# Kernel optimization log

Hardware: AMD Instinct MI355X
Metric: run time of the kernel (lower is better)

Reference implementation:

```python
import jax, jax.numpy as jnp
import numpy as np

SEQ = 2048
DIM = 2048
GROUPS = 8
GROUP_SIZE = 4
DQK = DIM // (GROUPS * GROUP_SIZE)  # 64 (also dim_v)


def _glorot(key, shape):
    # Faithful to source: dim_in = prod(shape[-1]) == shape[-1], so sigma = 1/sqrt(shape[-1])
    sigma = np.sqrt(2.0 / (shape[-1] + shape[-1])).astype(np.float32)
    return jax.random.normal(key, shape, dtype=jnp.float32) * sigma


def rope(x):
    """RoPE on last axis; x: [..., seq, dim]. Closed-form per-pair rotation."""
    seq, dim = x.shape[-2], x.shape[-1]
    half = dim // 2
    # angle[s, j] = s * 10000^(-2j/dim)
    inv_freq = 10000.0 ** (-2.0 * jnp.arange(half, dtype=jnp.float32) / dim)
    ang = jnp.arange(seq, dtype=jnp.float32)[:, None] * inv_freq[None, :]  # [seq, half]
    c, s = jnp.cos(ang), jnp.sin(ang)
    xp = x.reshape(*x.shape[:-1], half, 2)
    x1, x2 = xp[..., 0], xp[..., 1]
    out = jnp.stack([c * x1 - s * x2, s * x1 + c * x2], axis=-1)
    return out.reshape(x.shape)


def setup_inputs() -> dict:
    key = jax.random.key(0)
    kx, kq, kk, kv, ko = jax.random.split(key, 5)
    return {
        "x": jax.random.normal(kx, (SEQ, DIM), dtype=jnp.float32),
        "w_query": _glorot(kq, (GROUPS, GROUP_SIZE, DIM, DQK)),
        "w_key": _glorot(kk, (GROUPS, DIM, DQK)),
        "w_value": _glorot(kv, (GROUPS, DIM, DQK)),
        "w_out": _glorot(ko, (GROUPS, GROUP_SIZE, DQK, DIM)),
    }


def reference(x, w_query, w_key, w_value, w_out):
    seq = x.shape[0]
    dqk = w_query.shape[-1]
    # projections: g=groups, h=group_size (query heads per group)
    q = rope(jnp.einsum('sd,ghdk->ghsk', x, w_query))  # [g,h,seq,dqk]
    k = rope(jnp.einsum('sd,gdk->gsk', x, w_key))      # [g,seq,dqk]
    v = jnp.einsum('sd,gdv->gsv', x, w_value)          # [g,seq,dv]
    scores = jnp.einsum('ghsk,gtk->ghst', q, k) / jnp.sqrt(jnp.float32(dqk))
    causal = jnp.tril(jnp.ones((seq, seq), dtype=bool))  # log(tril(ones)) == 0 / -inf
    scores = jnp.where(causal, scores, -jnp.inf)
    probs = jax.nn.softmax(scores, axis=-1)
    o = jnp.einsum('ghst,gtv->ghsv', probs, v)
    # per-head out-proj then sum over (g, h)
    return jnp.einsum('ghsv,ghvd->sd', o, w_out)
```

## Files before the change

### kernel.cpp

```cpp
#include <hip/hip_runtime.h>
#include <hip/hip_bf16.h>

#define SEQ 2048
#define DIMM 2048
#define NQH 32
#define NKVH 8
#define HD 64

typedef _Float16 half8 __attribute__((ext_vector_type(8)));
typedef float f32x4 __attribute__((ext_vector_type(4)));
typedef __fp16 fp16raw2 __attribute__((ext_vector_type(2)));
using fp16 = _Float16;

typedef __attribute__((address_space(1))) unsigned int ga_u32;
typedef __attribute__((address_space(3))) unsigned int ls_u32;

__device__ __forceinline__ void gll16(const void* g, void* l) {
    __builtin_amdgcn_global_load_lds((const ga_u32*)g, (ls_u32*)l, 16, 0, 0);
}

__device__ __forceinline__ float fexp2(float x) {
#if __has_builtin(__builtin_amdgcn_exp2f)
    return __builtin_amdgcn_exp2f(x);
#else
    float r;
    asm("v_exp_f32 %0, %1" : "=v"(r) : "v"(x));
    return r;
#endif
}

__global__ void prep_kernel(const float* __restrict__ x,
                            const float* __restrict__ wq, const float* __restrict__ wk,
                            const float* __restrict__ wv, const float* __restrict__ wo,
                            fp16* __restrict__ xh, fp16* __restrict__ wqkvt,
                            fp16* __restrict__ w2t, float2* __restrict__ trig) {
    __shared__ float tile[64][65];
    const int bx = blockIdx.x;
    const int t = threadIdx.x;
    if (bx < 1024) {
#pragma unroll
        for (int it = 0; it < 4; it++) {
            int i = bx * 4096 + it * 1024 + t * 4;
            float4 v = *reinterpret_cast<const float4*>(x + i);
            fp16* o = xh + i;
            o[0] = (fp16)v.x; o[1] = (fp16)v.y; o[2] = (fp16)v.z; o[3] = (fp16)v.w;
        }
    } else if (bx < 2560) {
        const int zi = bx - 1024;
        const int z = zi >> 5;
        const int r0 = (zi & 31) * 64;
        const float* inh = (z < 32) ? wq + (size_t)z * SEQ * HD
                                    : (z < 40) ? wk + (size_t)(z - 32) * SEQ * HD
                                               : wv + (size_t)(z - 40) * SEQ * HD;
        fp16* outh = wqkvt + (size_t)z * HD * SEQ;
#pragma unroll
        for (int i = 0; i < 16; i++) {
            int idx = i * 256 + t;
            int r = idx >> 6, c = idx & 63;
            tile[r][c] = inh[(size_t)(r0 + r) * HD + c];
        }
        __syncthreads();
#pragma unroll
        for (int i = 0; i < 16; i++) {
            int idx = i * 256 + t;
            int cc = idx >> 6, rr = idx & 63;
            outh[(size_t)cc * SEQ + r0 + rr] = (fp16)tile[rr][cc];
        }
    } else if (bx < 3584) {
        const int zi = bx - 2560;
        const int r0 = (zi >> 5) * 64, c0 = (zi & 31) * 64;
#pragma unroll
        for (int i = 0; i < 16; i++) {
            int idx = i * 256 + t;
            int r = idx >> 6, c = idx & 63;
            tile[r][c] = wo[(size_t)(r0 + r) * 2048 + c0 + c];
        }
        __syncthreads();
#pragma unroll
        for (int i = 0; i < 16; i++) {
            int idx = i * 256 + t;
            int cc = idx >> 6, rr = idx & 63;
            w2t[(size_t)(c0 + cc) * 2048 + r0 + rr] = (fp16)tile[rr][cc];
        }
    } else {
        int idx = (bx - 3584) * 256 + t;
        int s = idx >> 5, j = idx & 31;
        float invf = expf(-0.28782313662425572f * (float)j);
        float sn, cs;
        sincosf((float)s * invf, &sn, &cs);
        trig[idx] = make_float2(cs, sn);
    }
}

__global__ __launch_bounds__(256) void gemm_qkv_fused(
    const fp16* __restrict__ A, const fp16* __restrict__ Bt, const float2* __restrict__ trig,
    fp16* __restrict__ qb, fp16* __restrict__ kb, fp16* __restrict__ vtb) {
    __shared__ fp16 As[2][64][64];
    __shared__ fp16 Bs[2][128][64];
    const int t = threadIdx.x;
    const int m0 = blockIdx.x * 64, n0 = blockIdx.y * 128;
    const int wid = t >> 6, lane = t & 63;
    const int wm = (wid >> 1) * 32, wn = (wid & 1) * 64;
    const int lr = lane & 15, lg = lane >> 4;
    f32x4 acc[2][4] = {};
    auto stage_ = [&](int kt, int b) {
#pragma unroll
        for (int s = t; s < 512; s += 256) {
            int row = s >> 3, ch = s & 7;
            int lch = ch ^ (row & 7);
            gll16(A + (size_t)(m0 + row) * 2048 + (kt << 6) + lch * 8,
                  (char*)&As[b][0][0] + s * 16);
        }
#pragma unroll
        for (int s = t; s < 1024; s += 256) {
            int row = s >> 3, ch = s & 7;
            int lch = ch ^ (row & 7);
            gll16(Bt + (size_t)(n0 + row) * 2048 + (kt << 6) + lch * 8,
                  (char*)&Bs[b][0][0] + s * 16);
        }
    };
    stage_(0, 0);
    __syncthreads();
    for (int kt = 0; kt < 32; ++kt) {
        const int cur = kt & 1;
        if (kt + 1 < 32) stage_(kt + 1, cur ^ 1);
#pragma unroll
        for (int kk = 0; kk < 2; kk++) {
            half8 af[2], bfv[4];
#pragma unroll
            for (int m = 0; m < 2; m++) {
                int row = wm + m * 16 + lr;
                af[m] = *(const half8*)((const char*)&As[cur][row][0] +
                                        (((kk * 4 + lg) ^ (row & 7)) * 16));
            }
#pragma unroll
            for (int n = 0; n < 4; n++) {
                int row = wn + n * 16 + lr;
                bfv[n] = *(const half8*)((const char*)&Bs[cur][row][0] +
                                         (((kk * 4 + lg) ^ (row & 7)) * 16));
            }
            __builtin_amdgcn_s_setprio(1);
#pragma unroll
            for (int m = 0; m < 2; m++)
#pragma unroll
                for (int n = 0; n < 4; n++)
                    acc[m][n] = __builtin_amdgcn_mfma_f32_16x16x32_f16(af[m], bfv[n], acc[m][n], 0, 0, 0);
            __builtin_amdgcn_s_setprio(0);
        }
        __syncthreads();
    }
    const int head0 = blockIdx.y * 2;
    if (head0 < 40) {
        const int head = head0 + (wid & 1);
        const float qscale = (head0 < 32) ? 0.18033688011112042f : 1.0f;
        fp16* outp = (head0 < 32) ? qb + (size_t)head * SEQ * HD
                                  : kb + (size_t)(head - 32) * SEQ * HD;
#pragma unroll
        for (int n = 0; n < 4; n++) {
            int c = n * 16 + lr;
            int j = c >> 1;
#pragma unroll
            for (int m = 0; m < 2; m++)
#pragma unroll
                for (int r = 0; r < 4; r++) {
                    int s = m0 + wm + m * 16 + lg * 4 + r;
                    float2 tc = trig[s * 32 + j];
                    float val = acc[m][n][r];
                    float pv = __shfl_xor(val, 1);
                    float o = (c & 1) ? (tc.y * pv + tc.x * val) : (tc.x * val - tc.y * pv);
                    outp[(size_t)s * HD + c] = (fp16)(o * qscale);
                }
        }
    } else {
        fp16* T = (fp16*)&Bs[0][0][0];
#pragma unroll
        for (int n = 0; n < 4; n++)
#pragma unroll
            for (int m = 0; m < 2; m++)
#pragma unroll
                for (int r = 0; r < 4; r++) {
                    int c = wn + n * 16 + lr;
                    int s = wm + m * 16 + lg * 4 + r;
                    T[c * 68 + s] = (fp16)acc[m][n][r];
                }
        __syncthreads();
        const int g0 = head0 - 40;
#pragma unroll
        for (int i = 0; i < 16; i++) {
            int idx = i * 256 + t;
            int c = idx >> 5, sp = (idx & 31) * 2;
            unsigned v = *(const unsigned*)&T[c * 68 + sp];
            *(unsigned*)(vtb + ((size_t)(g0 + (c >> 6)) * 64 + (c & 63)) * SEQ + m0 + sp) = v;
        }
    }
}

template <int BM, int BN, int WF32>
__global__ __launch_bounds__(256) void gemm_tpl(
    const fp16* __restrict__ A, const fp16* __restrict__ Bt, void* __restrict__ Cout, int Nout) {
    __shared__ fp16 As[2][BM][64];
    __shared__ fp16 Bs[2][BN][64];
    const int t = threadIdx.x;
    const int m0 = blockIdx.x * BM, n0 = blockIdx.y * BN;
    const int wid = t >> 6, lane = t & 63;
    const int wm = (wid >> 1) * (BM / 2), wn = (wid & 1) * (BN / 2);
    const int lr = lane & 15, lg = lane >> 4;
    constexpr int MR = BM / 32, NR = BN / 32;
    f32x4 acc[MR][NR] = {};
    auto stage_ = [&](int kt, int b) {
#pragma unroll
        for (int s = t; s < BM * 8; s += 256) {
            int row = s >> 3, ch = s & 7;
            int lch = ch ^ (row & 7);
            gll16(A + (size_t)(m0 + row) * 2048 + (kt << 6) + lch * 8,
                  (char*)&As[b][0][0] + s * 16);
        }
#pragma unroll
        for (int s = t; s < BN * 8; s += 256) {
            int row = s >> 3, ch = s & 7;
            int lch = ch ^ (row & 7);
            gll16(Bt + (size_t)(n0 + row) * 2048 + (kt << 6) + lch * 8,
                  (char*)&Bs[b][0][0] + s * 16);
        }
    };
    stage_(0, 0);
    __syncthreads();
    for (int kt = 0; kt < 32; ++kt) {
        const int cur = kt & 1;
        if (kt + 1 < 32) stage_(kt + 1, cur ^ 1);
#pragma unroll
        for (int kk = 0; kk < 2; kk++) {
            half8 af[MR], bfv[NR];
#pragma unroll
            for (int m = 0; m < MR; m++) {
                int row = wm + m * 16 + lr;
                af[m] = *(const half8*)((const char*)&As[cur][row][0] +
                                        (((kk * 4 + lg) ^ (row & 7)) * 16));
            }
#pragma unroll
            for (int n = 0; n < NR; n++) {
                int row = wn + n * 16 + lr;
                bfv[n] = *(const half8*)((const char*)&Bs[cur][row][0] +
                                         (((kk * 4 + lg) ^ (row & 7)) * 16));
            }
            __builtin_amdgcn_s_setprio(1);
#pragma unroll
            for (int m = 0; m < MR; m++)
#pragma unroll
                for (int n = 0; n < NR; n++)
                    acc[m][n] = __builtin_amdgcn_mfma_f32_16x16x32_f16(af[m], bfv[n], acc[m][n], 0, 0, 0);
            __builtin_amdgcn_s_setprio(0);
        }
        __syncthreads();
    }
#pragma unroll
    for (int m = 0; m < MR; m++)
#pragma unroll
        for (int n = 0; n < NR; n++)
#pragma unroll
            for (int r = 0; r < 4; r++) {
                int row = m0 + wm + m * 16 + lg * 4 + r;
                int col = n0 + wn + n * 16 + lr;
                if (WF32)
                    ((float*)Cout)[(size_t)row * Nout + col] = acc[m][n][r];
                else
                    ((fp16*)Cout)[(size_t)row * Nout + col] = (fp16)acc[m][n][r];
            }
}

__global__ __launch_bounds__(256) void attn_kernel(
    const fp16* __restrict__ qb, const fp16* __restrict__ kb,
    const fp16* __restrict__ vt, fp16* __restrict__ o_all) {
    __shared__ fp16 Kb[2][64][64];
    __shared__ fp16 Vb[2][64][64];
    __shared__ fp16 P[4][16][64];
    const int t = threadIdx.x, wid = t >> 6, lane = t & 63;
    const int bx = blockIdx.x;
    const int grp = bx >> 5;
    const int a = grp & 7;
    const int sel = grp >> 3;
    const int qt = (sel == 0) ? (31 - a) : (sel == 1) ? (8 + a) : (sel == 2) ? (23 - a) : a;
    const int head = bx & 31;
    const int g = head >> 2;
    const int lr = lane & 15, lg = lane >> 4;
    const fp16* qh = qb + (size_t)head * SEQ * HD;
    const fp16* kh = kb + (size_t)g * SEQ * HD;
    const fp16* vh = vt + (size_t)g * HD * SEQ;
    const int srow = lane >> 3, schunk = lane & 7;
    const int qr0 = qt * 64 + wid * 16;
    char* pb = (char*)&P[wid][0][0];

    half8 aq0 = *reinterpret_cast<const half8*>(qh + (size_t)(qr0 + lr) * HD + lg * 8);
    half8 aq1 = *reinterpret_cast<const half8*>(qh + (size_t)(qr0 + lr) * HD + 32 + lg * 8);
    f32x4 o[4] = {};
    float m_ = -1e30f, lsum_ = 0.0f;
    const int nt = qt + 1;

    const char* kga = (const char*)kh + (size_t)((wid * 16 + srow) * 64 + (schunk ^ srow) * 8) * 2;
    const char* vga = (const char*)vh + ((size_t)(wid * 16 + srow) * 2048 + (size_t)((schunk ^ srow) * 8)) * 2;
    char* kd0 = (char*)&Kb[0][wid * 16][0];
    char* vd0 = (char*)&Vb[0][wid * 16][0];
    int sb = 0;
    auto stage = [&]() {
        char* kdst = kd0 + sb * 8192;
        char* vdst = vd0 + sb * 8192;
        gll16(kga, kdst);
        gll16(kga + 1024, kdst + 1024);
        gll16(vga, vdst);
        gll16(vga + 32768, vdst + 1024);
        kga += 8192;
        vga += 128;
        sb ^= 1;
    };

    int koff[4][2];
#pragma unroll
    for (int f = 0; f < 4; f++) {
        int row = f * 16 + lr;
        koff[f][0] = row * 128 + ((lg ^ (row & 7)) * 16);
        koff[f][1] = row * 128 + (((4 + lg) ^ (row & 7)) * 16);
    }
    int voff[2][4];
#pragma unroll
    for (int h = 0; h < 2; h++)
#pragma unroll
        for (int vf = 0; vf < 4; vf++) {
            int d = vf * 16 + lr;
            voff[h][vf] = d * 128 + (((h * 4 + lg) ^ (d & 7)) * 16);
        }
    int pwoff[4];
#pragma unroll
    for (int f = 0; f < 4; f++) pwoff[f] = lr * 128 + ((f * 32 + lg * 8) ^ ((lr & 7) << 4));
    int proff[2];
#pragma unroll
    for (int h = 0; h < 2; h++) proff[h] = lr * 128 + (((h * 4 + lg) ^ (lr & 7)) * 16);

    stage();
    __syncthreads();
    for (int tt = 0; tt < nt; ++tt) {
        const int cur = tt & 1;
        if (tt + 1 < nt) stage();
        const int kv0 = tt << 6;
        const char* kbb = (const char*)&Kb[0][0][0] + cur * 8192;
        const char* vbb = (const char*)&Vb[0][0][0] + cur * 8192;
        f32x4 sc[4];
        __builtin_amdgcn_s_setprio(1);
#pragma unroll
        for (int f = 0; f < 4; ++f) {
            half8 b0 = *(const half8*)(kbb + koff[f][0]);
            half8 b1 = *(const half8*)(kbb + koff[f][1]);
            f32x4 s = {};
            s = __builtin_amdgcn_mfma_f32_16x16x32_f16(b0, aq0, s, 0, 0, 0);
            s = __builtin_amdgcn_mfma_f32_16x16x32_f16(b1, aq1, s, 0, 0, 0);
            sc[f] = s;
        }
        __builtin_amdgcn_s_setprio(0);
        if (tt == qt) {
            const int q = qr0 + lr;
#pragma unroll
            for (int f = 0; f < 4; f++)
#pragma unroll
                for (int r = 0; r < 4; r++) {
                    int kv = kv0 + f * 16 + lg * 4 + r;
                    if (kv > q) sc[f][r] = -1e30f;
                }
        }
        float t0 = fmaxf(fmaxf(sc[0][0], sc[0][1]), sc[0][2]);
        float t1 = fmaxf(fmaxf(sc[0][3], sc[1][0]), sc[1][1]);
        float t2 = fmaxf(fmaxf(sc[1][2], sc[1][3]), sc[2][0]);
        float t3 = fmaxf(fmaxf(sc[2][1], sc[2][2]), sc[2][3]);
        float t4 = fmaxf(fmaxf(sc[3][0], sc[3][1]), sc[3][2]);
        float lmax = fmaxf(fmaxf(fmaxf(t0, t1), t2), fmaxf(fmaxf(t3, t4), sc[3][3]));
        if (!__all(lmax <= m_ + 11.0f)) {
            float v = lmax;
            v = fmaxf(v, __shfl_xor(v, 16));
            v = fmaxf(v, __shfl_xor(v, 32));
            float mn = fmaxf(m_, v);
            float alpha = fexp2(m_ - mn);
            m_ = mn;
            lsum_ *= alpha;
            float al[4];
#pragma unroll
            for (int r = 0; r < 4; r++) al[r] = __shfl(alpha, lg * 4 + r);
#pragma unroll
            for (int vf = 0; vf < 4; vf++)
#pragma unroll
                for (int r = 0; r < 4; r++) o[vf][r] *= al[r];
        }
#pragma unroll
        for (int f = 0; f < 4; f++) {
            float p0 = fexp2(sc[f][0] - m_);
            float p1 = fexp2(sc[f][1] - m_);
            float p2 = fexp2(sc[f][2] - m_);
            float p3 = fexp2(sc[f][3] - m_);
            lsum_ += (p0 + p1) + (p2 + p3);
            fp16raw2 k0 = __builtin_amdgcn_cvt_pkrtz(p0, p1);
            fp16raw2 k1 = __builtin_amdgcn_cvt_pkrtz(p2, p3);
            uint2 w;
            w.x = __builtin_bit_cast(unsigned int, k0);
            w.y = __builtin_bit_cast(unsigned int, k1);
            *(uint2*)(pb + pwoff[f]) = w;
        }
        __builtin_amdgcn_s_setprio(1);
#pragma unroll
        for (int h = 0; h < 2; h++) {
            half8 pa = *(const half8*)(pb + proff[h]);
#pragma unroll
            for (int vf = 0; vf < 4; vf++) {
                half8 bv = *(const half8*)(vbb + voff[h][vf]);
                o[vf] = __builtin_amdgcn_mfma_f32_16x16x32_f16(pa, bv, o[vf], 0, 0, 0);
            }
        }
        __builtin_amdgcn_s_setprio(0);
        __syncthreads();
    }
    lsum_ += __shfl_xor(lsum_, 16);
    lsum_ += __shfl_xor(lsum_, 32);
    float li[4];
#pragma unroll
    for (int r = 0; r < 4; r++) li[r] = 1.0f / __shfl(lsum_, lg * 4 + r);
#pragma unroll
    for (int vf = 0; vf < 4; vf++)
#pragma unroll
        for (int r = 0; r < 4; r++) {
            float v = o[vf][r] * li[r];
            o_all[(size_t)(qr0 + lg * 4 + r) * 2048 + head * 64 + vf * 16 + lr] = (fp16)v;
        }
}

extern "C" void kernel_launch(void* const* d_in, const int* in_sizes, int n_in,
                              void* d_out, int out_size, void* d_ws, size_t ws_size,
                              hipStream_t stream) {
    const float* x  = (const float*)d_in[0];
    const float* wq = (const float*)d_in[1];
    const float* wk = (const float*)d_in[2];
    const float* wv = (const float*)d_in[3];
    const float* wo = (const float*)d_in[4];
    float* out = (float*)d_out;
    char* ws = (char*)d_ws;

    fp16*   xh    = (fp16*)(ws);
    fp16*   wqkvt = (fp16*)(ws + ((size_t)8 << 20));
    fp16*   o_all = (fp16*)(ws + ((size_t)20 << 20));
    fp16*   w2t   = (fp16*)(ws + ((size_t)28 << 20));
    fp16*   qbuf  = (fp16*)(ws + ((size_t)36 << 20));
    fp16*   kbuf  = (fp16*)(ws + ((size_t)44 << 20));
    fp16*   vtb   = (fp16*)(ws + ((size_t)46 << 20));
    float2* trig  = (float2*)(ws + ((size_t)48 << 20));

    prep_kernel<<<dim3(3840), 256, 0, stream>>>(x, wq, wk, wv, wo, xh, wqkvt, w2t, trig);
    gemm_qkv_fused<<<dim3(32, 24), 256, 0, stream>>>(xh, wqkvt, trig, qbuf, kbuf, vtb);
    attn_kernel<<<dim3(1024), 256, 0, stream>>>(qbuf, kbuf, vtb, o_all);
    gemm_tpl<64, 128, 1><<<dim3(32, 16), 256, 0, stream>>>(o_all, w2t, out, 2048);
}
```

Baseline: 122.1 us.

## Split long causal attention tiles into two KV partitions with a combine kernel

```diff
diff --git a/kernel.cpp b/kernel.cpp
--- a/kernel.cpp
+++ b/kernel.cpp
@@ -270,17 +270,27 @@
 
 __global__ __launch_bounds__(256) void attn_kernel(
     const fp16* __restrict__ qb, const fp16* __restrict__ kb,
-    const fp16* __restrict__ vt, fp16* __restrict__ o_all) {
+    const fp16* __restrict__ vt, fp16* __restrict__ o_all,
+    fp16* __restrict__ part_o, float* __restrict__ part_mlog) {
     __shared__ fp16 Kb[2][64][64];
     __shared__ fp16 Vb[2][64][64];
     __shared__ fp16 P[4][16][64];
     const int t = threadIdx.x, wid = t >> 6, lane = t & 63;
     const int bx = blockIdx.x;
-    const int grp = bx >> 5;
-    const int a = grp & 7;
-    const int sel = grp >> 3;
-    const int qt = (sel == 0) ? (31 - a) : (sel == 1) ? (8 + a) : (sel == 2) ? (23 - a) : a;
-    const int head = bx & 31;
+    int qt, head, t_lo, t_hi, slot, mode;
+    if (bx < 1024) {
+        qt = 31 - (bx >> 6);
+        head = (bx >> 1) & 31;
+        slot = bx & 1;
+        mode = 1;
+        if (slot == 0) { t_lo = 0; t_hi = 16; }
+        else           { t_lo = 16; t_hi = qt + 1; }
+    } else {
+        int i = bx - 1024;
+        qt = 15 - (i >> 5);
+        head = i & 31;
+        t_lo = 0; t_hi = qt + 1; slot = 0; mode = 0;
+    }
     const int g = head >> 2;
     const int lr = lane & 15, lg = lane >> 4;
     const fp16* qh = qb + (size_t)head * SEQ * HD;
@@ -294,10 +304,11 @@
     half8 aq1 = *reinterpret_cast<const half8*>(qh + (size_t)(qr0 + lr) * HD + 32 + lg * 8);
     f32x4 o[4] = {};
     float m_ = -1e30f, lsum_ = 0.0f;
-    const int nt = qt + 1;
-
-    const char* kga = (const char*)kh + (size_t)((wid * 16 + srow) * 64 + (schunk ^ srow) * 8) * 2;
-    const char* vga = (const char*)vh + ((size_t)(wid * 16 + srow) * 2048 + (size_t)((schunk ^ srow) * 8)) * 2;
+
+    const char* kga = (const char*)kh +
+        (size_t)((wid * 16 + srow) * 64 + (schunk ^ srow) * 8) * 2 + (size_t)t_lo * 8192;
+    const char* vga = (const char*)vh +
+        ((size_t)(wid * 16 + srow) * 2048 + (size_t)((schunk ^ srow) * 8)) * 2 + (size_t)t_lo * 128;
     char* kd0 = (char*)&Kb[0][wid * 16][0];
     char* vd0 = (char*)&Vb[0][wid * 16][0];
     int sb = 0;
@@ -337,9 +348,9 @@
 
     stage();
     __syncthreads();
-    for (int tt = 0; tt < nt; ++tt) {
-        const int cur = tt & 1;
-        if (tt + 1 < nt) stage();
+    for (int tt = t_lo; tt < t_hi; ++tt) {
+        const int cur = (tt - t_lo) & 1;
+        if (tt + 1 < t_hi) stage();
         const int kv0 = tt << 6;
         const char* kbb = (const char*)&Kb[0][0][0] + cur * 8192;
         const char* vbb = (const char*)&Vb[0][0][0] + cur * 8192;
@@ -419,13 +430,55 @@
     float li[4];
 #pragma unroll
     for (int r = 0; r < 4; r++) li[r] = 1.0f / __shfl(lsum_, lg * 4 + r);
-#pragma unroll
-    for (int vf = 0; vf < 4; vf++)
-#pragma unroll
-        for (int r = 0; r < 4; r++) {
-            float v = o[vf][r] * li[r];
-            o_all[(size_t)(qr0 + lg * 4 + r) * 2048 + head * 64 + vf * 16 + lr] = (fp16)v;
-        }
+    if (mode == 0) {
+#pragma unroll
+        for (int vf = 0; vf < 4; vf++)
+#pragma unroll
+            for (int r = 0; r < 4; r++) {
+                float v = o[vf][r] * li[r];
+                o_all[(size_t)(qr0 + lg * 4 + r) * 2048 + head * 64 + vf * 16 + lr] = (fp16)v;
+            }
+    } else {
+        const size_t sbase = ((size_t)((qt - 16) * 32 + head) * 2 + slot);
+        fp16* po = part_o + sbase * 4096;
+        float* pm = part_mlog + sbase * 64;
+#pragma unroll
+        for (int vf = 0; vf < 4; vf++)
+#pragma unroll
+            for (int r = 0; r < 4; r++) {
+                int rl = wid * 16 + lg * 4 + r;
+                po[rl * 64 + vf * 16 + lr] = (fp16)(o[vf][r] * li[r]);
+            }
+        if (lg == 0) pm[wid * 16 + lr] = m_ + __log2f(lsum_);
+    }
+}
+
+__global__ void attn_combine(const fp16* __restrict__ part_o, const float* __restrict__ part_mlog,
+                             fp16* __restrict__ o_all) {
+    const int bx = blockIdx.x;
+    const int head = bx & 31, qi = bx >> 5;
+    const int qt = 16 + qi;
+    const int t = threadIdx.x;
+    const int row = t >> 2, c0 = (t & 3) * 16;
+    const size_t base = (size_t)(qi * 32 + head) * 2;
+    const float m0 = part_mlog[(base + 0) * 64 + row];
+    const float m1 = part_mlog[(base + 1) * 64 + row];
+    const float M = fmaxf(m0, m1);
+    const float w0 = fexp2(m0 - M), w1 = fexp2(m1 - M);
+    const float inv = 1.0f / (w0 + w1);
+    const fp16* p0 = part_o + (base + 0) * 4096 + row * 64 + c0;
+    const fp16* p1 = part_o + (base + 1) * 4096 + row * 64 + c0;
+    fp16* dst = o_all + (size_t)(qt * 64 + row) * 2048 + head * 64 + c0;
+    half8 a0 = *(const half8*)p0, a1 = *(const half8*)(p0 + 8);
+    half8 b0 = *(const half8*)p1, b1 = *(const half8*)(p1 + 8);
+    half8 r0, r1;
+#pragma unroll
+    for (int j = 0; j < 8; j++) {
+        r0[j] = (fp16)((w0 * (float)a0[j] + w1 * (float)b0[j]) * inv);
+        r1[j] = (fp16)((w0 * (float)a1[j] + w1 * (float)b1[j]) * inv);
+    }
+    *(half8*)dst = r0;
+    *(half8*)(dst + 8) = r1;
 }
 
 extern "C" void kernel_launch(void* const* d_in, const int* in_sizes, int n_in,
@@ -439,17 +492,20 @@
     float* out = (float*)d_out;
     char* ws = (char*)d_ws;
 
-    fp16*   xh    = (fp16*)(ws);
-    fp16*   wqkvt = (fp16*)(ws + ((size_t)8 << 20));
-    fp16*   o_all = (fp16*)(ws + ((size_t)20 << 20));
-    fp16*   w2t   = (fp16*)(ws + ((size_t)28 << 20));
-    fp16*   qbuf  = (fp16*)(ws + ((size_t)36 << 20));
-    fp16*   kbuf  = (fp16*)(ws + ((size_t)44 << 20));
-    fp16*   vtb   = (fp16*)(ws + ((size_t)46 << 20));
-    float2* trig  = (float2*)(ws + ((size_t)48 << 20));
+    fp16*   xh        = (fp16*)(ws);
+    fp16*   wqkvt     = (fp16*)(ws + ((size_t)8 << 20));
+    fp16*   o_all     = (fp16*)(ws + ((size_t)20 << 20));
+    fp16*   w2t       = (fp16*)(ws + ((size_t)28 << 20));
+    fp16*   qbuf      = (fp16*)(ws + ((size_t)36 << 20));
+    fp16*   kbuf      = (fp16*)(ws + ((size_t)44 << 20));
+    fp16*   vtb       = (fp16*)(ws + ((size_t)46 << 20));
+    float2* trig      = (float2*)(ws + ((size_t)48 << 20));
+    fp16*   part_o    = (fp16*)(ws + ((size_t)49 << 20));
+    float*  part_mlog = (float*)(ws + ((size_t)57 << 20));
 
     prep_kernel<<<dim3(3840), 256, 0, stream>>>(x, wq, wk, wv, wo, xh, wqkvt, w2t, trig);
     gemm_qkv_fused<<<dim3(32, 24), 256, 0, stream>>>(xh, wqkvt, trig, qbuf, kbuf, vtb);
-    attn_kernel<<<dim3(1024), 256, 0, stream>>>(qbuf, kbuf, vtb, o_all);
+    attn_kernel<<<dim3(1536), 256, 0, stream>>>(qbuf, kbuf, vtb, o_all, part_o, part_mlog);
+    attn_combine<<<dim3(512), 256, 0, stream>>>(part_o, part_mlog, o_all);
     gemm_tpl<64, 128, 1><<<dim3(32, 16), 256, 0, stream>>>(o_all, w2t, out, 2048);
 }
```

New measurement: 132.9 us. 8.9% more time.
